# Performance work log

Measured on AMD Instinct MI355X. Metric: run time of the kernel, lower is better.

The kernel has to match this reference:

```python
import jax, jax.numpy as jnp
import numpy as np

T, B, F, H, P = 256, 512, 256, 512, 12  # seq len, batch, feature_dim, hidden_dim, p_interval


def setup_inputs() -> dict:
    key = jax.random.key(0)
    ks = jax.random.split(key, 9)
    s = 1.0 / np.sqrt(F + H)  # torch Linear default init scale
    def lin(k):
        kw, kb = jax.random.split(k)
        W = jax.random.uniform(kw, (F + H, H), jnp.float32, -s, s)
        b = jax.random.uniform(kb, (H,), jnp.float32, -s, s)
        return W, b
    Wf, bf = lin(ks[0])
    Wi, bi = lin(ks[1])
    Wo, bo = lin(ks[2])
    Wg, bg = lin(ks[3])
    x = jax.random.normal(ks[4], (T, B, F), jnp.float32)
    return {"x": x, "Wf": Wf, "bf": bf, "Wi": Wi, "bi": bi,
            "Wo": Wo, "bo": bo, "Wg": Wg, "bg": bg}


def _slstm(x, Wf, bf, Wi, bi, Wo, bo, Wg, bg):
    Tn, Bn, _ = x.shape
    h0 = jnp.zeros((P, Bn, H), x.dtype)
    # NOTE: original torch code reassigns c to a 2D [B,H] tensor after step 0,
    # so c[t % P] indexes a batch ROW (shape [H]) that broadcasts. At t=0 the
    # slice is all-zeros either way, so carrying a 2D c is exactly faithful.
    c0 = jnp.zeros((Bn, H), x.dtype)

    def step(carry, inp):
        h, c = carry
        x_t, t = inp
        idx = t % P
        xc = jnp.concatenate([x_t, h[idx]], axis=1)  # [B, F+H]
        f = jax.nn.softmax(xc @ Wf + bf, axis=1)
        i = jax.nn.softmax(xc @ Wi + bi, axis=1)
        o = jax.nn.softmax(xc @ Wo + bo, axis=1)
        g = jnp.tanh(xc @ Wg + bg)
        c_new = jnp.tanh(f * c[idx] + i * g)  # c[idx]: row [H], broadcasts over B
        h = h.at[idx].set(o * c_new)
        return (h, c_new), None

    (h, _), _ = jax.lax.scan(step, (h0, c0), (x, jnp.arange(Tn)))
    return h[(Tn - 1) % P]


def reference(x, Wf, bf, Wi, bi, Wo, bo, Wg, bg):
    return _slstm(x, Wf, bf, Wi, bi, Wo, bo, Wg, bg)
```

## Files before the change

kernel.cpp:

```cpp
#include <hip/hip_runtime.h>

typedef unsigned short u16;
typedef unsigned int   u32;

typedef __attribute__((ext_vector_type(8))) short bf16x8;
typedef __attribute__((ext_vector_type(4))) float f32x4;

__device__ __forceinline__ u16 f2bf(float v) {
    u32 u = __float_as_uint(v);
    u32 r = (u + 0x7fffu + ((u >> 16) & 1u)) >> 16;
    return (u16)r;
}
__device__ __forceinline__ float bf2f(u16 h) { return __uint_as_float(((u32)h) << 16); }

__device__ __forceinline__ void gl2lds16(const void* g, void* l) {
    __builtin_amdgcn_global_load_lds(
        (const __attribute__((address_space(1))) void*)g,
        (__attribute__((address_space(3))) void*)l, 16, 0, 0);
}

__global__ void init_k(u16* __restrict__ hh, u16* __restrict__ hl, float* __restrict__ rb) {
    int i = blockIdx.x * 256 + threadIdx.x;
    hh[i] = 0; hl[i] = 0;
    if (i < 13 * 512) rb[i] = 0.0f;
}

__global__ void pack_w(const float* __restrict__ Wf, const float* __restrict__ bf_,
                       const float* __restrict__ Wi, const float* __restrict__ bi_,
                       const float* __restrict__ Wo, const float* __restrict__ bo_,
                       const float* __restrict__ Wg, const float* __restrict__ bg_,
                       u16* __restrict__ wth, u16* __restrict__ wtl, float* __restrict__ bias4) {
    int idx = blockIdx.x * 256 + threadIdx.x;
    int n = idx / 768, k = idx - n * 768;
    int gate = n >> 9, col = n & 511;
    const float* W = (gate == 0) ? Wf : (gate == 1) ? Wi : (gate == 2) ? Wo : Wg;
    float v = W[k * 512 + col];
    u16 h = f2bf(v);
    wth[idx] = h;
    wtl[idx] = f2bf(v - bf2f(h));
    if (k == 0) {
        const float* bb = (gate == 0) ? bf_ : (gate == 1) ? bi_ : (gate == 2) ? bo_ : bg_;
        bias4[n] = bb[col];
    }
}

__global__ void split_x(const float* __restrict__ src, u16* __restrict__ oh, u16* __restrict__ ol) {
    int i = blockIdx.x * 256 + threadIdx.x;
    float4 v = ((const float4*)src)[i];
    u16 hx = f2bf(v.x), hy = f2bf(v.y), hz = f2bf(v.z), hw = f2bf(v.w);
    u16 lx = f2bf(v.x - bf2f(hx)), ly = f2bf(v.y - bf2f(hy));
    u16 lz = f2bf(v.z - bf2f(hz)), lw = f2bf(v.w - bf2f(hw));
    uint2 hv; hv.x = (u32)hx | ((u32)hy << 16); hv.y = (u32)hz | ((u32)hw << 16);
    uint2 lv; lv.x = (u32)lx | ((u32)ly << 16); lv.y = (u32)lz | ((u32)lw << 16);
    ((uint2*)oh)[i] = hv;
    ((uint2*)ol)[i] = lv;
}

#define BK 32
__global__ __launch_bounds__(256, 2) void gemm_x3(
    const u16* __restrict__ xh, const u16* __restrict__ xl,
    const u16* __restrict__ hh, const u16* __restrict__ hl,
    const u16* __restrict__ wth, const u16* __restrict__ wtl,
    const float* __restrict__ bias4, float* __restrict__ lg) {
    __shared__ __align__(16) u16 Ah[128 * BK];
    __shared__ __align__(16) u16 Al[128 * BK];
    __shared__ __align__(16) u16 Bh[128 * BK];
    __shared__ __align__(16) u16 Bl[128 * BK];

    const int tid = threadIdx.x;
    const int wid = tid >> 6, lane = tid & 63;
    const int bn = blockIdx.x, bm = blockIdx.y;
    const int s = bm >> 2;
    const int b0 = (bm & 3) * 128;
    const int laneR = lane >> 2;
    const int laneC = (lane & 3) * 8;

    u16* lds = (wid == 0) ? Ah : (wid == 1) ? Al : (wid == 2) ? Bh : Bl;
    const u16* xp = (wid == 0) ? xh : xl;
    const u16* hp = (wid == 0) ? hh : hl;
    const u16* wp = (wid == 2) ? wth : wtl;
    const u16* xrow = xp + (size_t)(s * 512 + b0) * 256 + laneR * 256 + laneC;
    const u16* hrow = hp + (size_t)(s * 512 + b0) * 512 + laneR * 512 + laneC;
    const u16* wrow = wp + (size_t)(bn * 128) * 768 + laneR * 768 + laneC;

    const int wm = wid >> 1, wn = wid & 1;
    const int lm = lane & 15, quad = lane >> 4;

    f32x4 acc[4][4];
#pragma unroll
    for (int i = 0; i < 4; i++)
#pragma unroll
        for (int j = 0; j < 4; j++) { acc[i][j].x = 0.f; acc[i][j].y = 0.f; acc[i][j].z = 0.f; acc[i][j].w = 0.f; }

    for (int k0 = 0; k0 < 768; k0 += BK) {
        __syncthreads();
        if (wid < 2) {
            if (k0 < 256) {
                const u16* src = xrow + k0;
#pragma unroll
                for (int r = 0; r < 8; ++r) gl2lds16(src + r * 16 * 256, lds + r * 16 * BK);
            } else {
                const u16* src = hrow + (k0 - 256);
#pragma unroll
                for (int r = 0; r < 8; ++r) gl2lds16(src + r * 16 * 512, lds + r * 16 * BK);
            }
        } else {
            const u16* src = wrow + k0;
#pragma unroll
            for (int r = 0; r < 8; ++r) gl2lds16(src + r * 16 * 768, lds + r * 16 * BK);
        }
        __syncthreads();

        bf16x8 a_h[4], a_l[4], b_h[4], b_l[4];
#pragma unroll
        for (int i = 0; i < 4; ++i) {
            a_h[i] = *(const bf16x8*)&Ah[(wm * 64 + i * 16 + lm) * BK + quad * 8];
            a_l[i] = *(const bf16x8*)&Al[(wm * 64 + i * 16 + lm) * BK + quad * 8];
            b_h[i] = *(const bf16x8*)&Bh[(wn * 64 + i * 16 + lm) * BK + quad * 8];
            b_l[i] = *(const bf16x8*)&Bl[(wn * 64 + i * 16 + lm) * BK + quad * 8];
        }
#pragma unroll
        for (int i = 0; i < 4; ++i)
#pragma unroll
            for (int j = 0; j < 4; ++j) {
                acc[i][j] = __builtin_amdgcn_mfma_f32_16x16x32_bf16(a_h[i], b_h[j], acc[i][j], 0, 0, 0);
                acc[i][j] = __builtin_amdgcn_mfma_f32_16x16x32_bf16(a_h[i], b_l[j], acc[i][j], 0, 0, 0);
                acc[i][j] = __builtin_amdgcn_mfma_f32_16x16x32_bf16(a_l[i], b_h[j], acc[i][j], 0, 0, 0);
            }
    }

#pragma unroll
    for (int j = 0; j < 4; ++j) {
        int n = bn * 128 + wn * 64 + j * 16 + lm;
        float bv = bias4[n];
#pragma unroll
        for (int i = 0; i < 4; ++i) {
            int row = wm * 64 + i * 16 + quad * 4;
            size_t base = (size_t)(bm * 128 + row) * 2048 + n;
#pragma unroll
            for (int r = 0; r < 4; ++r) lg[base + (size_t)r * 2048] = acc[i][j][r] + bv;
        }
    }
}

__global__ void chain_k(const float* __restrict__ lg, float* __restrict__ rb, int S) {
    const int lane = threadIdx.x;
    float r[8];
#pragma unroll
    for (int u = 0; u < 8; ++u) r[u] = rb[12 * 512 + lane * 8 + u];
    for (int s = 0; s < S; ++s) {
#pragma unroll
        for (int u = 0; u < 8; ++u) rb[s * 512 + lane * 8 + u] = r[u];
        int rowb = (s + 1) % 12;
        const float* base = lg + (size_t)(s * 512 + rowb) * 2048 + lane * 8;
        float f[8], iv[8], g[8];
#pragma unroll
        for (int u = 0; u < 8; ++u) { f[u] = base[u]; iv[u] = base[512 + u]; g[u] = base[1536 + u]; }
        float mf = -1e30f, mi = -1e30f;
#pragma unroll
        for (int u = 0; u < 8; ++u) { mf = fmaxf(mf, f[u]); mi = fmaxf(mi, iv[u]); }
#pragma unroll
        for (int o = 32; o; o >>= 1) { mf = fmaxf(mf, __shfl_xor(mf, o)); mi = fmaxf(mi, __shfl_xor(mi, o)); }
        float sf = 0.f, si = 0.f;
#pragma unroll
        for (int u = 0; u < 8; ++u) {
            f[u] = __expf(f[u] - mf); sf += f[u];
            iv[u] = __expf(iv[u] - mi); si += iv[u];
        }
#pragma unroll
        for (int o = 32; o; o >>= 1) { sf += __shfl_xor(sf, o); si += __shfl_xor(si, o); }
        float rf = 1.0f / sf, ri = 1.0f / si;
#pragma unroll
        for (int u = 0; u < 8; ++u) {
            float gg = tanhf(g[u]);
            r[u] = tanhf(f[u] * rf * r[u] + iv[u] * ri * gg);
        }
    }
#pragma unroll
    for (int u = 0; u < 8; ++u) rb[12 * 512 + lane * 8 + u] = r[u];
}

__global__ __launch_bounds__(256) void gates_k(
    const float* __restrict__ lg, const float* __restrict__ rb,
    u16* __restrict__ hh, u16* __restrict__ hl,
    float* __restrict__ out, int t0) {
    const int w = (blockIdx.x * 256 + threadIdx.x) >> 6;
    const int lane = threadIdx.x & 63;
    const int s = w >> 9, b = w & 511;
    const int t = t0 + s;
    const float* row = lg + (size_t)(s * 512 + b) * 2048 + lane * 8;
    float f[8], iv[8], ov[8], g[8];
#pragma unroll
    for (int u = 0; u < 8; ++u) {
        f[u] = row[u]; iv[u] = row[512 + u]; ov[u] = row[1024 + u]; g[u] = row[1536 + u];
    }
    float mf = -1e30f, mi = -1e30f, mo = -1e30f;
#pragma unroll
    for (int u = 0; u < 8; ++u) { mf = fmaxf(mf, f[u]); mi = fmaxf(mi, iv[u]); mo = fmaxf(mo, ov[u]); }
#pragma unroll
    for (int o = 32; o; o >>= 1) {
        mf = fmaxf(mf, __shfl_xor(mf, o));
        mi = fmaxf(mi, __shfl_xor(mi, o));
        mo = fmaxf(mo, __shfl_xor(mo, o));
    }
    float sf = 0.f, si = 0.f, so = 0.f;
#pragma unroll
    for (int u = 0; u < 8; ++u) {
        f[u] = __expf(f[u] - mf); sf += f[u];
        iv[u] = __expf(iv[u] - mi); si += iv[u];
        ov[u] = __expf(ov[u] - mo); so += ov[u];
    }
#pragma unroll
    for (int o = 32; o; o >>= 1) {
        sf += __shfl_xor(sf, o); si += __shfl_xor(si, o); so += __shfl_xor(so, o);
    }
    float rf = 1.0f / sf, ri = 1.0f / si, ro = 1.0f / so;
    float hout[8];
#pragma unroll
    for (int u = 0; u < 8; ++u) {
        float rr = rb[s * 512 + lane * 8 + u];
        float gg = tanhf(g[u]);
        float cv = tanhf(f[u] * rf * rr + iv[u] * ri * gg);
        hout[u] = ov[u] * ro * cv;
    }
    u32 hhp[4], hlp[4];
#pragma unroll
    for (int u = 0; u < 4; ++u) {
        u16 h0 = f2bf(hout[2 * u]), h1 = f2bf(hout[2 * u + 1]);
        u16 l0 = f2bf(hout[2 * u] - bf2f(h0)), l1 = f2bf(hout[2 * u + 1] - bf2f(h1));
        hhp[u] = (u32)h0 | ((u32)h1 << 16);
        hlp[u] = (u32)l0 | ((u32)l1 << 16);
    }
    size_t hb = ((size_t)(s * 512 + b)) * 512 + lane * 8;
    *(uint4*)&hh[hb] = make_uint4(hhp[0], hhp[1], hhp[2], hhp[3]);
    *(uint4*)&hl[hb] = make_uint4(hlp[0], hlp[1], hlp[2], hlp[3]);
    if (t == 255) {
        float* op = out + (size_t)b * 512 + lane * 8;
#pragma unroll
        for (int u = 0; u < 8; ++u) op[u] = hout[u];
    }
}

extern "C" void kernel_launch(void* const* d_in, const int* in_sizes, int n_in,
                              void* d_out, int out_size, void* d_ws, size_t ws_size,
                              hipStream_t stream) {
    const float* x   = (const float*)d_in[0];
    const float* Wf  = (const float*)d_in[1];
    const float* bf_ = (const float*)d_in[2];
    const float* Wi  = (const float*)d_in[3];
    const float* bi_ = (const float*)d_in[4];
    const float* Wo  = (const float*)d_in[5];
    const float* bo_ = (const float*)d_in[6];
    const float* Wg  = (const float*)d_in[7];
    const float* bg_ = (const float*)d_in[8];
    float* out = (float*)d_out;

    char* p = (char*)d_ws;
    u16* xh  = (u16*)p; p += 3145728;
    u16* xl  = (u16*)p; p += 3145728;
    u16* wth = (u16*)p; p += 3145728;
    u16* wtl = (u16*)p; p += 3145728;
    u16* hh  = (u16*)p; p += 6291456;
    u16* hl  = (u16*)p; p += 6291456;
    float* bias4 = (float*)p; p += 8192;
    float* rb    = (float*)p; p += 32768;
    float* lg    = (float*)p; p += 50331648;

    init_k<<<12288, 256, 0, stream>>>(hh, hl, rb);
    pack_w<<<6144, 256, 0, stream>>>(Wf, bf_, Wi, bi_, Wo, bo_, Wg, bg_, wth, wtl, bias4);

    for (int blk = 0; blk < 22; ++blk) {
        int t0 = blk * 12;
        int S = (256 - t0 >= 12) ? 12 : (256 - t0);
        split_x<<<S * 128, 256, 0, stream>>>(x + (size_t)t0 * 512 * 256, xh, xl);
        gemm_x3<<<dim3(16, S * 4), 256, 0, stream>>>(xh, xl, hh, hl, wth, wtl, bias4, lg);
        chain_k<<<1, 64, 0, stream>>>(lg, rb, S);
        gates_k<<<S * 128, 256, 0, stream>>>(lg, rb, hh, hl, out, t0);
    }
}
```

Before: 2.400 ms.

## Fold serial c-row chain into gates kernel and hoist x split out of loop

Removes the single-wavefront chain_k launch per block. Each gates block now recomputes the broadcast c-row recurrence up to its own step into shared memory, and the last block advances the carry into a double-buffered buffer for the next block. The bf16 hi/lo split of x is done once for the whole sequence before the loop instead of once per 12-step block, which cuts launches but needs a much larger workspace. It also raises the gemm occupancy hint from 2 to 3, and it adds redundant serial work in every gates block, up to 11 chain steps.

```diff
diff --git a/kernel.cpp b/kernel.cpp
--- a/kernel.cpp
+++ b/kernel.cpp
@@ -19,10 +19,10 @@
         (__attribute__((address_space(3))) void*)l, 16, 0, 0);
 }
 
-__global__ void init_k(u16* __restrict__ hh, u16* __restrict__ hl, float* __restrict__ rb) {
+__global__ void init_k(u16* __restrict__ hh, u16* __restrict__ hl, float* __restrict__ cb) {
     int i = blockIdx.x * 256 + threadIdx.x;
     hh[i] = 0; hl[i] = 0;
-    if (i < 13 * 512) rb[i] = 0.0f;
+    if (i < 2 * 512) cb[i] = 0.0f;
 }
 
 __global__ void pack_w(const float* __restrict__ Wf, const float* __restrict__ bf_,
@@ -57,7 +57,7 @@
 }
 
 #define BK 32
-__global__ __launch_bounds__(256, 2) void gemm_x3(
+__global__ __launch_bounds__(256, 3) void gemm_x3(
     const u16* __restrict__ xh, const u16* __restrict__ xl,
     const u16* __restrict__ hh, const u16* __restrict__ hl,
     const u16* __restrict__ wth, const u16* __restrict__ wtl,
@@ -143,51 +143,58 @@
     }
 }
 
-__global__ void chain_k(const float* __restrict__ lg, float* __restrict__ rb, int S) {
-    const int lane = threadIdx.x;
-    float r[8];
-#pragma unroll
-    for (int u = 0; u < 8; ++u) r[u] = rb[12 * 512 + lane * 8 + u];
-    for (int s = 0; s < S; ++s) {
-#pragma unroll
-        for (int u = 0; u < 8; ++u) rb[s * 512 + lane * 8 + u] = r[u];
-        int rowb = (s + 1) % 12;
-        const float* base = lg + (size_t)(s * 512 + rowb) * 2048 + lane * 8;
-        float f[8], iv[8], g[8];
-#pragma unroll
-        for (int u = 0; u < 8; ++u) { f[u] = base[u]; iv[u] = base[512 + u]; g[u] = base[1536 + u]; }
-        float mf = -1e30f, mi = -1e30f;
-#pragma unroll
-        for (int u = 0; u < 8; ++u) { mf = fmaxf(mf, f[u]); mi = fmaxf(mi, iv[u]); }
-#pragma unroll
-        for (int o = 32; o; o >>= 1) { mf = fmaxf(mf, __shfl_xor(mf, o)); mi = fmaxf(mi, __shfl_xor(mi, o)); }
-        float sf = 0.f, si = 0.f;
-#pragma unroll
-        for (int u = 0; u < 8; ++u) {
-            f[u] = __expf(f[u] - mf); sf += f[u];
-            iv[u] = __expf(iv[u] - mi); si += iv[u];
-        }
-#pragma unroll
-        for (int o = 32; o; o >>= 1) { sf += __shfl_xor(sf, o); si += __shfl_xor(si, o); }
-        float rf = 1.0f / sf, ri = 1.0f / si;
-#pragma unroll
-        for (int u = 0; u < 8; ++u) {
-            float gg = tanhf(g[u]);
-            r[u] = tanhf(f[u] * rf * r[u] + iv[u] * ri * gg);
-        }
-    }
-#pragma unroll
-    for (int u = 0; u < 8; ++u) rb[12 * 512 + lane * 8 + u] = r[u];
+__device__ __forceinline__ void chain_step(const float* __restrict__ lg, int j, int lane, float r[8]) {
+    int rowb = (j + 1) % 12;
+    const float* base = lg + (size_t)(j * 512 + rowb) * 2048 + lane * 8;
+    float f[8], iv[8], g[8];
+#pragma unroll
+    for (int u = 0; u < 8; ++u) { f[u] = base[u]; iv[u] = base[512 + u]; g[u] = base[1536 + u]; }
+    float mf = -1e30f, mi = -1e30f;
+#pragma unroll
+    for (int u = 0; u < 8; ++u) { mf = fmaxf(mf, f[u]); mi = fmaxf(mi, iv[u]); }
+#pragma unroll
+    for (int o = 32; o; o >>= 1) { mf = fmaxf(mf, __shfl_xor(mf, o)); mi = fmaxf(mi, __shfl_xor(mi, o)); }
+    float sf = 0.f, si = 0.f;
+#pragma unroll
+    for (int u = 0; u < 8; ++u) {
+        f[u] = __expf(f[u] - mf); sf += f[u];
+        iv[u] = __expf(iv[u] - mi); si += iv[u];
+    }
+#pragma unroll
+    for (int o = 32; o; o >>= 1) { sf += __shfl_xor(sf, o); si += __shfl_xor(si, o); }
+    float rf = 1.0f / sf, ri = 1.0f / si;
+#pragma unroll
+    for (int u = 0; u < 8; ++u) {
+        float gg = tanhf(g[u]);
+        r[u] = tanhf(f[u] * rf * r[u] + iv[u] * ri * gg);
+    }
 }
 
 __global__ __launch_bounds__(256) void gates_k(
-    const float* __restrict__ lg, const float* __restrict__ rb,
+    const float* __restrict__ lg, float* __restrict__ cb,
     u16* __restrict__ hh, u16* __restrict__ hl,
-    float* __restrict__ out, int t0) {
-    const int w = (blockIdx.x * 256 + threadIdx.x) >> 6;
-    const int lane = threadIdx.x & 63;
-    const int s = w >> 9, b = w & 511;
+    float* __restrict__ out, int t0, int S, int rd, int wr) {
+    __shared__ float rsh[512];
+    const int widx = threadIdx.x >> 6, lane = threadIdx.x & 63;
+    const int s = blockIdx.x >> 7;
+    const int b = (blockIdx.x & 127) * 4 + widx;
     const int t = t0 + s;
+
+    if (widx == 0) {
+        float r[8];
+#pragma unroll
+        for (int u = 0; u < 8; ++u) r[u] = cb[rd * 512 + lane * 8 + u];
+        for (int j = 0; j < s; ++j) chain_step(lg, j, lane, r);
+#pragma unroll
+        for (int u = 0; u < 8; ++u) rsh[lane * 8 + u] = r[u];
+        if ((int)blockIdx.x == S * 128 - 1 && t0 + S < 256) {
+            chain_step(lg, s, lane, r);
+#pragma unroll
+            for (int u = 0; u < 8; ++u) cb[wr * 512 + lane * 8 + u] = r[u];
+        }
+    }
+    __syncthreads();
+
     const float* row = lg + (size_t)(s * 512 + b) * 2048 + lane * 8;
     float f[8], iv[8], ov[8], g[8];
 #pragma unroll
@@ -218,7 +225,7 @@
     float hout[8];
 #pragma unroll
     for (int u = 0; u < 8; ++u) {
-        float rr = rb[s * 512 + lane * 8 + u];
+        float rr = rsh[lane * 8 + u];
         float gg = tanhf(g[u]);
         float cv = tanhf(f[u] * rf * rr + iv[u] * ri * gg);
         hout[u] = ov[u] * ro * cv;
@@ -256,25 +263,26 @@
     float* out = (float*)d_out;
 
     char* p = (char*)d_ws;
-    u16* xh  = (u16*)p; p += 3145728;
-    u16* xl  = (u16*)p; p += 3145728;
+    u16* xh  = (u16*)p; p += 134217728;
+    u16* xl  = (u16*)p; p += 134217728;
     u16* wth = (u16*)p; p += 3145728;
     u16* wtl = (u16*)p; p += 3145728;
     u16* hh  = (u16*)p; p += 6291456;
     u16* hl  = (u16*)p; p += 6291456;
     float* bias4 = (float*)p; p += 8192;
-    float* rb    = (float*)p; p += 32768;
+    float* cb    = (float*)p; p += 4096;
     float* lg    = (float*)p; p += 50331648;
 
-    init_k<<<12288, 256, 0, stream>>>(hh, hl, rb);
+    init_k<<<12288, 256, 0, stream>>>(hh, hl, cb);
     pack_w<<<6144, 256, 0, stream>>>(Wf, bf_, Wi, bi_, Wo, bo_, Wg, bg_, wth, wtl, bias4);
+    split_x<<<32768, 256, 0, stream>>>(x, xh, xl);
 
     for (int blk = 0; blk < 22; ++blk) {
         int t0 = blk * 12;
         int S = (256 - t0 >= 12) ? 12 : (256 - t0);
-        split_x<<<S * 128, 256, 0, stream>>>(x + (size_t)t0 * 512 * 256, xh, xl);
-        gemm_x3<<<dim3(16, S * 4), 256, 0, stream>>>(xh, xl, hh, hl, wth, wtl, bias4, lg);
-        chain_k<<<1, 64, 0, stream>>>(lg, rb, S);
-        gates_k<<<S * 128, 256, 0, stream>>>(lg, rb, hh, hl, out, t0);
-    }
-}
+        gemm_x3<<<dim3(16, S * 4), 256, 0, stream>>>(
+            xh + (size_t)t0 * 512 * 256, xl + (size_t)t0 * 512 * 256,
+            hh, hl, wth, wtl, bias4, lg);
+        gates_k<<<S * 128, 256, 0, stream>>>(lg, cb, hh, hl, out, t0, S, blk & 1, (blk + 1) & 1);
+    }
+}
```

Measured after the change: 2.154 ms. 10.3% less time.
